# Kernel optimization log

Measured on AMD Instinct MI355X. Metric: run time of the kernel, lower is better.

## Reference

```python
import jax, jax.numpy as jnp
import numpy as np

D_MODEL, D_K, D_V = 1024, 128, 128
B, S = 8, 2048


def setup_inputs() -> dict:
    key = jax.random.key(0)
    k1, k2, k3, k4, k5 = jax.random.split(key, 5)
    x = jax.random.normal(k1, (B, S, D_MODEL), dtype=jnp.float32)
    enc_embed = jax.random.normal(k2, (B, S, D_MODEL), dtype=jnp.float32)
    # xavier_normal-ish init: std = sqrt(2/(fan_in+fan_out))
    W_Q = jax.random.normal(k3, (D_MODEL, D_K), dtype=jnp.float32) * np.sqrt(2.0 / (D_MODEL + D_K))
    W_K = jax.random.normal(k4, (D_MODEL, D_K), dtype=jnp.float32) * np.sqrt(2.0 / (D_MODEL + D_K))
    W_V = jax.random.normal(k5, (D_MODEL, D_V), dtype=jnp.float32) * np.sqrt(2.0 / (D_MODEL + D_V))
    return {"x": x, "enc_embed": enc_embed, "W_Q": W_Q, "W_K": W_K, "W_V": W_V}


def reference(x, enc_embed, W_Q, W_K, W_V):
    # use_enc_embed=False, use_mask=False path (self-attention)
    q = jnp.einsum('bsd,dk->bsk', x, W_Q)  # [B,S,d_k]
    k = jnp.einsum('bsd,dk->bsk', x, W_K)  # [B,S,d_k]
    v = jnp.einsum('bsd,dv->bsv', x, W_V)  # [B,S,d_v]
    scale = 1.0 / jnp.sqrt(jnp.asarray(D_K, dtype=x.dtype))
    scores = jnp.einsum('bqk,bsk->bqs', q, k) * scale  # [B,S,S]
    weights = jax.nn.softmax(scores, axis=-1)
    return jnp.einsum('bqs,bsv->bqv', weights, v)  # [B,S,d_v]
```

## Files before the change

kernel.cpp:

```cpp
#include <hip/hip_runtime.h>
#include <hip/hip_bf16.h>
#include <stdint.h>

typedef __attribute__((ext_vector_type(8))) short bf16x8;
typedef __attribute__((ext_vector_type(4))) float f32x4;
typedef __attribute__((ext_vector_type(4))) unsigned short u16x4;
typedef unsigned short u16;

#define D_MODEL 1024
#define DK 128
#define BATCH 8
#define SEQ 2048
#define NROWS (BATCH * SEQ)
#define NSPLIT 4
#define KVPB 512
#define NIT 16

static __device__ __forceinline__ void gl_lds16(const void* g, void* l) {
  __builtin_amdgcn_global_load_lds((const __attribute__((address_space(1))) void*)g,
                                   (__attribute__((address_space(3))) void*)l, 16, 0, 0);
}

static __device__ __forceinline__ u16 f2b(float f) {
  __hip_bfloat16 h = __float2bfloat16(f);
  return *reinterpret_cast<u16*>(&h);
}

static __device__ __forceinline__ uint32_t cvtpk(float lo, float hi) {
  uint32_t r;
  asm("v_cvt_pk_bf16_f32 %0, %1, %2" : "=v"(r) : "v"(lo), "v"(hi));
  return r;
}

static __device__ __forceinline__ float exp2hw(float x) {
  float r;
  asm("v_exp_f32 %0, %1" : "=v"(r) : "v"(x));
  return r;
}

__global__ __launch_bounds__(256) void wcvt(const float* __restrict__ wq,
                                            const float* __restrict__ wk,
                                            const float* __restrict__ wv,
                                            u16* __restrict__ wt) {
  const int idx = blockIdx.x * 256 + threadIdx.x;
  int w = idx >> 17, rr = idx & 131071, k = rr >> 7, n = rr & 127;
  const float* W = (w == 0) ? wq : ((w == 1) ? wk : wv);
  wt[(size_t)w * 131072 + (size_t)n * 1024 + k] = f2b(W[k * DK + n]);
}

__global__ __launch_bounds__(256, 3) void qkv_gemm(const float* __restrict__ x,
                                                   const u16* __restrict__ wt,
                                                   u16* __restrict__ qb,
                                                   u16* __restrict__ kb,
                                                   u16* __restrict__ vt) {
  __shared__ char sm[49152] __attribute__((aligned(16)));
  const int tid = threadIdx.x;
  const int lane = tid & 63;
  const int w = tid >> 6;
  const int g = lane >> 4;
  const int l15 = lane & 15;
  const int id = blockIdx.x;
  const int wg = (id & 7) * 96 + (id >> 3);
  const int mt = wg / 3;
  const int nt = wg - mt * 3;
  const int wm = w >> 1, wn = w & 1;

  const char* aB = (const char*)x + (size_t)mt * 64 * 4096;
  const char* bB = (const char*)wt + (size_t)nt * 262144;

  f32x4 acc[2][4];
#pragma unroll
  for (int i = 0; i < 2; ++i)
#pragma unroll
    for (int jj = 0; jj < 4; ++jj) acc[i][jj] = (f32x4){0.f, 0.f, 0.f, 0.f};

  auto stage = [&](int buf, int kt) {
    char* sA = sm + buf * 16384;
    char* sB = sA + 8192;
#pragma unroll
    for (int c = 0; c < 2; ++c) {
      int L = c * 4096 + tid * 16;
      {
        int row = L >> 7;
        int gq = ((L >> 4) & 7) ^ (row & 7);
        gl_lds16(aB + (size_t)row * 4096 + kt * 128 + (gq << 4),
                 sA + c * 4096 + w * 1024);
      }
      {
        int n = L >> 6;
        int cq = ((L >> 4) & 3) ^ ((n >> 1) & 3);
        gl_lds16(bB + (size_t)n * 2048 + kt * 64 + (cq << 4),
                 sB + c * 4096 + w * 1024);
      }
    }
  };

  auto compute = [&](const char* base) {
    const char* sA = base;
    const char* sB = base + 8192;
    bf16x8 af[2];
#pragma unroll
    for (int mi = 0; mi < 2; ++mi) {
      int row = wm * 32 + mi * 16 + l15;
      f32x4 lo = *(const f32x4*)(sA + row * 128 + ((((2 * g + 0) ^ (row & 7))) << 4));
      f32x4 hi = *(const f32x4*)(sA + row * 128 + ((((2 * g + 1) ^ (row & 7))) << 4));
      union { uint32_t u[4]; bf16x8 v; } t;
      t.u[0] = cvtpk(lo[0], lo[1]);
      t.u[1] = cvtpk(lo[2], lo[3]);
      t.u[2] = cvtpk(hi[0], hi[1]);
      t.u[3] = cvtpk(hi[2], hi[3]);
      af[mi] = t.v;
    }
    bf16x8 bfr[4];
#pragma unroll
    for (int ni = 0; ni < 4; ++ni) {
      int n = wn * 64 + ni * 16 + l15;
      bfr[ni] = *(const bf16x8*)(sB + n * 64 + ((g ^ ((n >> 1) & 3)) << 4));
    }
    __builtin_amdgcn_s_setprio(1);
#pragma unroll
    for (int mi = 0; mi < 2; ++mi)
#pragma unroll
      for (int ni = 0; ni < 4; ++ni)
        acc[mi][ni] = __builtin_amdgcn_mfma_f32_16x16x32_bf16(af[mi], bfr[ni], acc[mi][ni], 0, 0, 0);
    __builtin_amdgcn_s_setprio(0);
  };

  stage(0, 0);
  stage(1, 1);
  int cb = 0;
#pragma unroll 1
  for (int t = 0; t < 32; ++t) {
    if (t < 31) asm volatile("s_waitcnt vmcnt(4)" ::: "memory");
    else asm volatile("s_waitcnt vmcnt(0)" ::: "memory");
    __builtin_amdgcn_s_barrier();
    if (t + 2 < 32) {
      int sb = cb + 2;
      if (sb >= 3) sb -= 3;
      stage(sb, t + 2);
    }
    compute(sm + cb * 16384);
    cb = (cb == 2) ? 0 : cb + 1;
  }

  const float qscale = 0.12751743f;
#pragma unroll
  for (int mi = 0; mi < 2; ++mi) {
#pragma unroll
    for (int ni = 0; ni < 4; ++ni) {
      int mbase = mt * 64 + wm * 32 + mi * 16 + g * 4;
      int n = wn * 64 + ni * 16 + l15;
      if (nt == 2) {
        int b = mbase >> 11, s = mbase & 2047;
        int a = (s >> 2) & 7;
        int sp2 = (s & ~31) | ((((a & 3) << 1) | (a >> 2)) << 2);
        union { u16 u[4]; u16x4 v; } pk;
#pragma unroll
        for (int r2 = 0; r2 < 4; ++r2) pk.u[r2] = f2b(acc[mi][ni][r2]);
        *(u16x4*)((char*)vt + ((size_t)(b * 128 + n) * 2048 + sp2) * 2) = pk.v;
      } else {
        u16* dst = (nt == 0) ? qb : kb;
        float sc = (nt == 0) ? qscale : 1.0f;
#pragma unroll
        for (int r2 = 0; r2 < 4; ++r2)
          dst[(size_t)(mbase + r2) * 128 + n] = f2b(acc[mi][ni][r2] * sc);
      }
    }
  }
}

__global__ __launch_bounds__(256) void attn(const u16* __restrict__ qb,
                                            const u16* __restrict__ kb,
                                            const u16* __restrict__ vtg,
                                            u16* __restrict__ po,
                                            float* __restrict__ ls) {
  __shared__ char sm[49152] __attribute__((aligned(16)));
  const int tid = threadIdx.x, lane = tid & 63, w = tid >> 6;
  const int g = lane >> 4, l15 = lane & 15;
  const int id = blockIdx.x;
  const int wgid = ((id & 7) << 6) | (id >> 3);
  const int b = wgid >> 6, sp = (wgid >> 4) & 3, j = wgid & 15;
  const int s0q = j * 128 + w * 32;
  const int kv0 = sp * KVPB;

  const char* qB = (const char*)qb + (size_t)b * SEQ * 256;
  const char* kB = (const char*)kb + (size_t)b * SEQ * 256;
  const char* vB = (const char*)vtg + (size_t)b * 128 * SEQ * 2;

  bf16x8 qf[2][4];
#pragma unroll
  for (int h = 0; h < 2; ++h)
#pragma unroll
    for (int kk = 0; kk < 4; ++kk)
      qf[h][kk] = *(const bf16x8*)(qB + (size_t)(s0q + h * 16 + l15) * 256 + kk * 64 + g * 16);

  f32x4 o[2][8];
#pragma unroll
  for (int h = 0; h < 2; ++h)
#pragma unroll
    for (int i = 0; i < 8; ++i) o[h][i] = (f32x4){0.f, 0.f, 0.f, 0.f};
  float lsum[2] = {0.f, 0.f};

  char* sKb = sm;
  char* sVb = sm + 24576;

  auto stage = [&](int bi, int it) {
    char* sK = sKb + bi * 8192;
    char* sV = sVb + bi * 8192;
    int s0 = kv0 + it * 32;
#pragma unroll
    for (int c = 0; c < 2; ++c) {
      int base = c * 4096 + w * 1024;
      int L = base + lane * 16;
      {
        int row = L >> 8, col = L & 255;
        gl_lds16(kB + (size_t)(s0 + row) * 256 + (col ^ ((row & 7) << 4)), sK + base);
      }
      {
        int rv = L >> 6, cv = L & 63;
        gl_lds16(vB + (size_t)rv * 4096 + (size_t)s0 * 2 + (cv ^ ((rv & 3) << 4)), sV + base);
      }
    }
  };

  stage(0, 0);
  stage(1, 1);
  int cb = 0;
  for (int t = 0; t < NIT; ++t) {
    if (t < NIT - 1) asm volatile("s_waitcnt vmcnt(4)" ::: "memory");
    else asm volatile("s_waitcnt vmcnt(0)" ::: "memory");
    __builtin_amdgcn_s_barrier();
    if (t + 2 < NIT) {
      int sb = cb + 2;
      if (sb >= 3) sb -= 3;
      stage(sb, t + 2);
    }
    const char* sK = sKb + cb * 8192;
    const char* sV = sVb + cb * 8192;

    f32x4 st[2][2];
    st[0][0] = (f32x4){0.f, 0.f, 0.f, 0.f}; st[0][1] = st[0][0];
    st[1][0] = st[0][0]; st[1][1] = st[0][0];
    __builtin_amdgcn_s_setprio(1);
#pragma unroll
    for (int sub = 0; sub < 2; ++sub)
#pragma unroll
      for (int kk = 0; kk < 4; ++kk) {
        bf16x8 kf = *(const bf16x8*)(sK + (sub * 16 + l15) * 256 +
                                     ((kk * 64 + g * 16) ^ ((l15 & 7) << 4)));
        st[0][sub] = __builtin_amdgcn_mfma_f32_16x16x32_bf16(kf, qf[0][kk], st[0][sub], 0, 0, 0);
        st[1][sub] = __builtin_amdgcn_mfma_f32_16x16x32_bf16(kf, qf[1][kk], st[1][sub], 0, 0, 0);
      }
    __builtin_amdgcn_s_setprio(0);

    union U { uint32_t u[4]; bf16x8 v; } pf[2];
#pragma unroll
    for (int h = 0; h < 2; ++h) {
      float p[8];
#pragma unroll
      for (int sub = 0; sub < 2; ++sub)
#pragma unroll
        for (int r2 = 0; r2 < 4; ++r2) {
          float e = exp2hw(st[h][sub][r2]);
          lsum[h] += e;
          p[sub * 4 + r2] = e;
        }
      pf[h].u[0] = cvtpk(p[0], p[1]);
      pf[h].u[1] = cvtpk(p[2], p[3]);
      pf[h].u[2] = cvtpk(p[4], p[5]);
      pf[h].u[3] = cvtpk(p[6], p[7]);
    }

    __builtin_amdgcn_s_setprio(1);
#pragma unroll
    for (int dsub = 0; dsub < 8; ++dsub) {
      bf16x8 vf = *(const bf16x8*)(sV + (dsub * 16 + l15) * 64 +
                                   ((g * 16) ^ ((l15 & 3) << 4)));
      o[0][dsub] = __builtin_amdgcn_mfma_f32_16x16x32_bf16(vf, pf[0].v, o[0][dsub], 0, 0, 0);
      o[1][dsub] = __builtin_amdgcn_mfma_f32_16x16x32_bf16(vf, pf[1].v, o[1][dsub], 0, 0, 0);
    }
    __builtin_amdgcn_s_setprio(0);
    cb = (cb == 2) ? 0 : cb + 1;
  }

#pragma unroll
  for (int h = 0; h < 2; ++h) {
    lsum[h] += __shfl_xor(lsum[h], 16);
    lsum[h] += __shfl_xor(lsum[h], 32);
    int ridx = (b * 16 + j) * 128 + w * 32 + h * 16 + l15;
    u16* dst = po + ((size_t)sp * NROWS + ridx) * 128;
#pragma unroll
    for (int dsub = 0; dsub < 8; ++dsub) {
      union { uint32_t u[2]; u16x4 v; } pk2;
      pk2.u[0] = cvtpk(o[h][dsub][0], o[h][dsub][1]);
      pk2.u[1] = cvtpk(o[h][dsub][2], o[h][dsub][3]);
      *(u16x4*)(dst + dsub * 16 + g * 4) = pk2.v;
    }
    if (g == 0) ls[(size_t)sp * NROWS + ridx] = lsum[h];
  }
}

__global__ __launch_bounds__(256) void attn_combine(const u16* __restrict__ po,
                                                    const float* __restrict__ ls,
                                                    float* __restrict__ out) {
  int idx = blockIdx.x * 256 + threadIdx.x;
  int r = idx >> 4, d0 = (idx & 15) * 8;
  float denom = 0.f;
  float acc[8];
#pragma unroll
  for (int j = 0; j < 8; ++j) acc[j] = 0.f;
#pragma unroll
  for (int s = 0; s < NSPLIT; ++s) {
    denom += ls[(size_t)s * NROWS + r];
    bf16x8 v = *(const bf16x8*)(po + ((size_t)s * NROWS + r) * 128 + d0);
#pragma unroll
    for (int j = 0; j < 8; ++j) {
      uint32_t bits = ((uint32_t)(u16)v[j]) << 16;
      acc[j] += *reinterpret_cast<float*>(&bits);
    }
  }
  float inv = 1.0f / denom;
  f32x4 o0 = (f32x4){acc[0], acc[1], acc[2], acc[3]};
  f32x4 o1 = (f32x4){acc[4], acc[5], acc[6], acc[7]};
  *(f32x4*)(out + (size_t)r * 128 + d0) = o0 * inv;
  *(f32x4*)(out + (size_t)r * 128 + d0 + 4) = o1 * inv;
}

extern "C" void kernel_launch(void* const* d_in, const int* in_sizes, int n_in,
                              void* d_out, int out_size, void* d_ws, size_t ws_size,
                              hipStream_t stream) {
  const float* x = (const float*)d_in[0];
  const float* wq = (const float*)d_in[2];
  const float* wk = (const float*)d_in[3];
  const float* wv = (const float*)d_in[4];

  char* ws = (char*)d_ws;
  u16* po = (u16*)ws;
  float* ls = (float*)(ws + 16777216);
  u16* wt = (u16*)(ws + 17039360);
  u16* qb = (u16*)(ws + 17825792);
  u16* kb = (u16*)(ws + 22020096);
  u16* vt = (u16*)(ws + 26214400);
  float* out = (float*)d_out;

  wcvt<<<dim3(1536), dim3(256), 0, stream>>>(wq, wk, wv, wt);
  qkv_gemm<<<dim3(768), dim3(256), 0, stream>>>(x, wt, qb, kb, vt);
  attn<<<dim3(512), dim3(256), 0, stream>>>(qb, kb, vt, po, ls);
  attn_combine<<<dim3(1024), dim3(256), 0, stream>>>(po, ls, out);
}
```

Baseline: 67.55 us.

## Compute all of Q, K, V per block to load x once

Measured after the change: 62.94 us. 1.07x faster.

```diff
diff --git a/kernel.cpp b/kernel.cpp
--- a/kernel.cpp
+++ b/kernel.cpp
@@ -48,50 +48,45 @@
   wt[(size_t)w * 131072 + (size_t)n * 1024 + k] = f2b(W[k * DK + n]);
 }
 
-__global__ __launch_bounds__(256, 3) void qkv_gemm(const float* __restrict__ x,
+__global__ __launch_bounds__(512, 1) void qkv_gemm(const float* __restrict__ x,
                                                    const u16* __restrict__ wt,
                                                    u16* __restrict__ qb,
                                                    u16* __restrict__ kb,
                                                    u16* __restrict__ vt) {
-  __shared__ char sm[49152] __attribute__((aligned(16)));
+  __shared__ char sm[98304] __attribute__((aligned(16)));
   const int tid = threadIdx.x;
   const int lane = tid & 63;
   const int w = tid >> 6;
   const int g = lane >> 4;
   const int l15 = lane & 15;
-  const int id = blockIdx.x;
-  const int wg = (id & 7) * 96 + (id >> 3);
-  const int mt = wg / 3;
-  const int nt = wg - mt * 3;
-  const int wm = w >> 1, wn = w & 1;
+  const int mt = blockIdx.x;
+  const int wm = w >> 2, wn = w & 3;
 
   const char* aB = (const char*)x + (size_t)mt * 64 * 4096;
-  const char* bB = (const char*)wt + (size_t)nt * 262144;
-
-  f32x4 acc[2][4];
+
+  f32x4 acc[2][6];
 #pragma unroll
   for (int i = 0; i < 2; ++i)
 #pragma unroll
-    for (int jj = 0; jj < 4; ++jj) acc[i][jj] = (f32x4){0.f, 0.f, 0.f, 0.f};
+    for (int jj = 0; jj < 6; ++jj) acc[i][jj] = (f32x4){0.f, 0.f, 0.f, 0.f};
 
   auto stage = [&](int buf, int kt) {
-    char* sA = sm + buf * 16384;
+    char* sA = sm + buf * 32768;
     char* sB = sA + 8192;
-#pragma unroll
-    for (int c = 0; c < 2; ++c) {
-      int L = c * 4096 + tid * 16;
-      {
-        int row = L >> 7;
-        int gq = ((L >> 4) & 7) ^ (row & 7);
-        gl_lds16(aB + (size_t)row * 4096 + kt * 128 + (gq << 4),
-                 sA + c * 4096 + w * 1024);
-      }
-      {
-        int n = L >> 6;
-        int cq = ((L >> 4) & 3) ^ ((n >> 1) & 3);
-        gl_lds16(bB + (size_t)n * 2048 + kt * 64 + (cq << 4),
-                 sB + c * 4096 + w * 1024);
-      }
+    {
+      int row = tid >> 3;
+      int gq = (tid & 7) ^ (row & 7);
+      gl_lds16(aB + (size_t)row * 4096 + kt * 128 + (gq << 4), sA + w * 1024);
+    }
+#pragma unroll
+    for (int c = 0; c < 3; ++c) {
+      int idx = c * 512 + tid;
+      int np = idx >> 2;
+      int cq = (idx & 3) ^ ((np >> 1) & 3);
+      gl_lds16((const char*)wt +
+                   ((size_t)(np >> 7) * 131072 + (size_t)(np & 127) * 1024) * 2 +
+                   kt * 64 + (cq << 4),
+               sB + c * 8192 + w * 1024);
     }
   };
 
@@ -104,24 +99,24 @@
       int row = wm * 32 + mi * 16 + l15;
       f32x4 lo = *(const f32x4*)(sA + row * 128 + ((((2 * g + 0) ^ (row & 7))) << 4));
       f32x4 hi = *(const f32x4*)(sA + row * 128 + ((((2 * g + 1) ^ (row & 7))) << 4));
-      union { uint32_t u[4]; bf16x8 v; } t;
-      t.u[0] = cvtpk(lo[0], lo[1]);
-      t.u[1] = cvtpk(lo[2], lo[3]);
-      t.u[2] = cvtpk(hi[0], hi[1]);
-      t.u[3] = cvtpk(hi[2], hi[3]);
-      af[mi] = t.v;
-    }
-    bf16x8 bfr[4];
-#pragma unroll
-    for (int ni = 0; ni < 4; ++ni) {
-      int n = wn * 64 + ni * 16 + l15;
-      bfr[ni] = *(const bf16x8*)(sB + n * 64 + ((g ^ ((n >> 1) & 3)) << 4));
+      union { uint32_t u[4]; bf16x8 v; } tt;
+      tt.u[0] = cvtpk(lo[0], lo[1]);
+      tt.u[1] = cvtpk(lo[2], lo[3]);
+      tt.u[2] = cvtpk(hi[0], hi[1]);
+      tt.u[3] = cvtpk(hi[2], hi[3]);
+      af[mi] = tt.v;
+    }
+    bf16x8 bfr[6];
+#pragma unroll
+    for (int ni = 0; ni < 6; ++ni) {
+      int np = wn * 96 + ni * 16 + l15;
+      bfr[ni] = *(const bf16x8*)(sB + np * 64 + ((g ^ ((np >> 1) & 3)) << 4));
     }
     __builtin_amdgcn_s_setprio(1);
 #pragma unroll
     for (int mi = 0; mi < 2; ++mi)
 #pragma unroll
-      for (int ni = 0; ni < 4; ++ni)
+      for (int ni = 0; ni < 6; ++ni)
         acc[mi][ni] = __builtin_amdgcn_mfma_f32_16x16x32_bf16(af[mi], bfr[ni], acc[mi][ni], 0, 0, 0);
     __builtin_amdgcn_s_setprio(0);
   };
@@ -139,7 +134,7 @@
       if (sb >= 3) sb -= 3;
       stage(sb, t + 2);
     }
-    compute(sm + cb * 16384);
+    compute(sm + cb * 32768);
     cb = (cb == 2) ? 0 : cb + 1;
   }
 
@@ -147,10 +142,11 @@
 #pragma unroll
   for (int mi = 0; mi < 2; ++mi) {
 #pragma unroll
-    for (int ni = 0; ni < 4; ++ni) {
+    for (int ni = 0; ni < 6; ++ni) {
       int mbase = mt * 64 + wm * 32 + mi * 16 + g * 4;
-      int n = wn * 64 + ni * 16 + l15;
-      if (nt == 2) {
+      int np = wn * 96 + ni * 16 + l15;
+      int ntd = np >> 7, n = np & 127;
+      if (ntd == 2) {
         int b = mbase >> 11, s = mbase & 2047;
         int a = (s >> 2) & 7;
         int sp2 = (s & ~31) | ((((a & 3) << 1) | (a >> 2)) << 2);
@@ -159,8 +155,8 @@
         for (int r2 = 0; r2 < 4; ++r2) pk.u[r2] = f2b(acc[mi][ni][r2]);
         *(u16x4*)((char*)vt + ((size_t)(b * 128 + n) * 2048 + sp2) * 2) = pk.v;
       } else {
-        u16* dst = (nt == 0) ? qb : kb;
-        float sc = (nt == 0) ? qscale : 1.0f;
+        u16* dst = (ntd == 0) ? qb : kb;
+        float sc = (ntd == 0) ? qscale : 1.0f;
 #pragma unroll
         for (int r2 = 0; r2 < 4; ++r2)
           dst[(size_t)(mbase + r2) * 128 + n] = f2b(acc[mi][ni][r2] * sc);
@@ -344,7 +340,7 @@
   float* out = (float*)d_out;
 
   wcvt<<<dim3(1536), dim3(256), 0, stream>>>(wq, wk, wv, wt);
-  qkv_gemm<<<dim3(768), dim3(256), 0, stream>>>(x, wt, qb, kb, vt);
+  qkv_gemm<<<dim3(256), dim3(512), 0, stream>>>(x, wt, qb, kb, vt);
   attn<<<dim3(512), dim3(256), 0, stream>>>(qb, kb, vt, po, ls);
   attn_combine<<<dim3(1024), dim3(256), 0, stream>>>(po, ls, out);
 }
```
